# Kernel optimization log

Hardware: AMD Instinct MI355X
Metric: run time of the kernel (lower is better)

## Reference

```python
import jax, jax.numpy as jnp
import numpy as np

VOCAB = 50257
EMB = 256
HID = 256
FORGET_BIAS = 1.0


def setup_inputs() -> dict:
    key = jax.random.key(0)
    ks = jax.random.split(key, 8)
    B, T = 16, 256
    s = 0.05
    return {
        "tokens": jax.random.randint(ks[0], (B, T), 0, VOCAB, dtype=jnp.int32),
        # embedding matrix init mimics tf.random_uniform(-1, 1)
        "emb": jax.random.uniform(ks[1], (VOCAB, EMB), jnp.float32, -1.0, 1.0),
        "W1": jax.random.normal(ks[2], (EMB + HID, 4 * HID), jnp.float32) * s,
        "b1": jnp.zeros((4 * HID,), jnp.float32),
        "W2": jax.random.normal(ks[3], (HID + HID, 4 * HID), jnp.float32) * s,
        "b2": jnp.zeros((4 * HID,), jnp.float32),
        "Wout": jax.random.normal(ks[4], (HID, VOCAB), jnp.float32) * s,
        "bout": jnp.zeros((VOCAB,), jnp.float32),
    }


def _lstm_cell(c, h, x, W, b):
    # BasicLSTMCell: gates = [x, h] @ W + b, split i, j, f, o
    g = jnp.concatenate([x, h], axis=-1) @ W + b
    i, j, f, o = jnp.split(g, 4, axis=-1)
    c_new = c * jax.nn.sigmoid(f + FORGET_BIAS) + jax.nn.sigmoid(i) * jnp.tanh(j)
    h_new = jnp.tanh(c_new) * jax.nn.sigmoid(o)
    return c_new, h_new


def reference(tokens, emb, W1, b1, W2, b2, Wout, bout):
    B, T = tokens.shape
    x = emb[tokens]                 # [B, T, EMB] embedding lookup
    x_tm = jnp.swapaxes(x, 0, 1)    # [T, B, EMB] time-major for scan

    def step(carry, xt):
        c1, h1, c2, h2 = carry
        c1, h1 = _lstm_cell(c1, h1, xt, W1, b1)
        c2, h2 = _lstm_cell(c2, h2, h1, W2, b2)
        return (c1, h1, c2, h2), h2

    z = jnp.zeros((B, HID), x.dtype)
    _, hs = jax.lax.scan(step, (z, z, z, z), x_tm)  # hs: [T, B, HID]
    hs = jnp.swapaxes(hs, 0, 1).reshape(-1, HID)    # [B*T, HID] (batch-major flatten as in tf.reshape)
    logits = hs @ Wout + bout                        # [B*T, VOCAB]
    return logits
```

## Files before the change

kernel.cpp:

```cpp
#include <hip/hip_runtime.h>
#include <hip/hip_bf16.h>
#include <stdint.h>

#define BB 16
#define TT 256
#define HH 256
#define EE 256
#define GG 1024
#define VV 50257
#define NPAD 50688
#define NN 4096

typedef unsigned short u16;
typedef __attribute__((ext_vector_type(8))) short short8;
typedef __attribute__((ext_vector_type(4))) float f32x4;

__device__ __forceinline__ float sigm(float x){
    float e = __builtin_amdgcn_exp2f(fminf(-x*1.44269504f, 60.0f));
    return 1.0f/(1.0f+e);
}
__device__ __forceinline__ float tanha(float x){
    float e = __builtin_amdgcn_exp2f(fminf(x*2.885390082f, 60.0f));
    return (e-1.0f)/(e+1.0f);
}
__device__ __forceinline__ u16 f2bf(float f){
    uint32_t u = __float_as_uint(f);
    u = (u + 0x7FFFu + ((u>>16)&1u)) >> 16;
    return (u16)u;
}
__device__ __forceinline__ void st32_coh(uint32_t* p, uint32_t v){
    __hip_atomic_store(p, v, __ATOMIC_RELAXED, __HIP_MEMORY_SCOPE_AGENT);
}
__device__ __forceinline__ uint32_t poll_pair(const uint32_t* p){
    uint32_t v = __hip_atomic_load(p, __ATOMIC_RELAXED, __HIP_MEMORY_SCOPE_AGENT);
    while ((v & 0xFFFFu) == 0xFFFFu || (v >> 16) == 0xFFFFu){
        __builtin_amdgcn_s_sleep(1);
        v = __hip_atomic_load(p, __ATOMIC_RELAXED, __HIP_MEMORY_SCOPE_AGENT);
    }
    return v;
}
__device__ __forceinline__ void gl_lds16(const void* g, void* s){
    __builtin_amdgcn_global_load_lds((const __attribute__((address_space(1))) unsigned int*)g,
                                     (__attribute__((address_space(3))) unsigned int*)s, 16, 0, 0);
}

__global__ __launch_bounds__(256) void g1_kernel(const int* __restrict__ tok, const float* __restrict__ emb,
                                                 const float* __restrict__ W1, const float* __restrict__ b1,
                                                 float* __restrict__ G1t){
    __shared__ float xs[64*64];
    __shared__ float wsm[64*64];
    int n0 = blockIdx.x * 64;
    int g0 = blockIdx.y * 64;
    int tid = threadIdx.x;
    int sl = tid & 63;
    int kk = (tid >> 6) * 16;
    int mytok = tok[n0 + sl];
    float acc[4][4] = {};
    int ni = tid & 15, gi = tid >> 4;
    for (int kc = 0; kc < 4; ++kc){
        int k0 = kc*64;
        __syncthreads();
        #pragma unroll
        for (int i4 = 0; i4 < 4; ++i4){
            float4 xv = *(const float4*)(&emb[(size_t)mytok*EE + k0 + kk + i4*4]);
            xs[(kk+i4*4+0)*64 + sl] = xv.x;
            xs[(kk+i4*4+1)*64 + sl] = xv.y;
            xs[(kk+i4*4+2)*64 + sl] = xv.z;
            xs[(kk+i4*4+3)*64 + sl] = xv.w;
        }
        #pragma unroll
        for (int i = 0; i < 16; ++i){
            wsm[(kk+i)*64 + sl] = W1[(size_t)(k0+kk+i)*GG + g0 + sl];
        }
        __syncthreads();
        for (int k = 0; k < 64; ++k){
            float4 av = *(const float4*)(&xs[k*64 + ni*4]);
            float4 bv = *(const float4*)(&wsm[k*64 + gi*4]);
            float a_[4] = {av.x, av.y, av.z, av.w};
            float b_[4] = {bv.x, bv.y, bv.z, bv.w};
            #pragma unroll
            for (int i = 0; i < 4; ++i)
                #pragma unroll
                for (int j = 0; j < 4; ++j)
                    acc[i][j] += a_[i]*b_[j];
        }
    }
    #pragma unroll
    for (int i = 0; i < 4; ++i){
        int n = n0 + ni*4 + i;
        int b = n >> 8;
        int tt_ = n & 255;
        float4 o;
        o.x = acc[i][0] + b1[g0+gi*4+0];
        o.y = acc[i][1] + b1[g0+gi*4+1];
        o.z = acc[i][2] + b1[g0+gi*4+2];
        o.w = acc[i][3] + b1[g0+gi*4+3];
        *(float4*)(&G1t[(size_t)(tt_*16 + b)*GG + g0 + gi*4]) = o;
    }
}

__global__ __launch_bounds__(1024) void persist_kernel(
        const float* __restrict__ G1t, const float* __restrict__ W1,
        const float* __restrict__ W2, const float* __restrict__ b2,
        const float* __restrict__ Wout, u16* __restrict__ WoutT,
        u16* __restrict__ h1y, u16* __restrict__ h2b){
    __shared__ __align__(16) char smem[12288];
    const int bid = blockIdx.x;
    const int tid = threadIdx.x;

    if (bid >= 96){
        u16* tile = (u16*)smem;
        const int r = tid >> 4, i = tid & 15;
        for (int tau = bid - 96; tau < 792*4; tau += 128){
            int ky = tau / 792;
            int nx = tau - ky*792;
            int n0 = nx*64, k0 = ky*64;
            #pragma unroll
            for (int jj = 0; jj < 4; ++jj){
                int n = n0 + i*4 + jj;
                float f = (n < VV) ? Wout[(size_t)(k0 + r)*VV + n] : 0.0f;
                tile[(i*4 + jj)*66 + r] = f2bf(f);
            }
            __syncthreads();
            {
                int kl = i*4;
                uint2 v;
                v.x = (uint32_t)tile[r*66 + kl+0] | ((uint32_t)tile[r*66 + kl+1] << 16);
                v.y = (uint32_t)tile[r*66 + kl+2] | ((uint32_t)tile[r*66 + kl+3] << 16);
                *(uint2*)(&WoutT[(size_t)(n0 + r)*256 + k0 + kl]) = v;
            }
            __syncthreads();
        }
        return;
    }

    const int g  = bid & 7;
    const int rr = bid >> 3;
    const int l  = tid & 63;
    const int wv = tid >> 6;
    uint32_t* h1y32 = (uint32_t*)h1y;
    uint32_t* h2b32 = (uint32_t*)h2b;

    if (rr < 4){
        const int r1 = rr;
        const int gate = wv >> 2, usub = wv & 3;
        const int colw = gate*HH + 64*r1 + 16*usub;
        short8 wf[8];
        {
            const int col = colw + (l & 15);
            const int kb = (l >> 4) << 3;
            #pragma unroll
            for (int kk = 0; kk < 8; ++kk){
                short8 s;
                #pragma unroll
                for (int j = 0; j < 8; ++j)
                    s[j] = (short)f2bf(W1[(size_t)(HH + kk*32 + kb + j)*GG + col]);
                wf[kk] = s;
            }
        }
        u16*      hA   = (u16*)smem;
        uint32_t* hA32 = (uint32_t*)smem;
        float*    gm   = (float*)(smem + 1024);
        const int ab = tid >> 5, ap_ = tid & 31;
        float creg0 = 0.f, creg1 = 0.f;

        for (int t = 0; t < TT; ++t){
            float c0 = 0.f, c1 = 0.f;
            if (l < 16){
                c0 = G1t[((size_t)t*BB + 2*g + 0)*GG + colw + l];
                c1 = G1t[((size_t)t*BB + 2*g + 1)*GG + colw + l];
            }
            f32x4 acc = {c0, c1, 0.f, 0.f};
            if (t > 0){
                if (tid < 256){
                    int b = tid >> 7, p = tid & 127;
                    hA32[b*128 + p] = poll_pair(&h1y32[(((size_t)(t-1)*8 + g)*2 + b)*128 + p]);
                }
                __syncthreads();
                const u16* app = hA + (l & 1)*256 + ((l >> 4) << 3);
                f32x4 acc2 = {0.f, 0.f, 0.f, 0.f};
                #pragma unroll
                for (int kk = 0; kk < 4; ++kk){
                    acc  = __builtin_amdgcn_mfma_f32_16x16x32_bf16(*(const short8*)(app + (2*kk  )*32), wf[2*kk  ], acc , 0, 0, 0);
                    acc2 = __builtin_amdgcn_mfma_f32_16x16x32_bf16(*(const short8*)(app + (2*kk+1)*32), wf[2*kk+1], acc2, 0, 0, 0);
                }
                acc[0] += acc2[0];
                acc[1] += acc2[1];
            }
            if (l < 16){
                gm[(gate*64 + usub*16 + l)*2 + 0] = acc[0];
                gm[(gate*64 + usub*16 + l)*2 + 1] = acc[1];
            }
            __syncthreads();
            if (tid < 64){
                int u0 = 2*ap_, u1 = 2*ap_ + 1;
                float gi0 = gm[(0*64 + u0)*2 + ab], gi1 = gm[(0*64 + u1)*2 + ab];
                float gj0 = gm[(1*64 + u0)*2 + ab], gj1 = gm[(1*64 + u1)*2 + ab];
                float gf0 = gm[(2*64 + u0)*2 + ab], gf1 = gm[(2*64 + u1)*2 + ab];
                float go0 = gm[(3*64 + u0)*2 + ab], go1 = gm[(3*64 + u1)*2 + ab];
                float cn0 = creg0 * sigm(gf0 + 1.0f) + sigm(gi0)*tanha(gj0);
                float cn1 = creg1 * sigm(gf1 + 1.0f) + sigm(gi1)*tanha(gj1);
                float hn0 = tanha(cn0)*sigm(go0);
                float hn1 = tanha(cn1)*sigm(go1);
                creg0 = cn0; creg1 = cn1;
                uint32_t pk = (uint32_t)f2bf(hn0) | ((uint32_t)f2bf(hn1) << 16);
                st32_coh(&h1y32[(((size_t)t*8 + g)*2 + ab)*128 + 32*r1 + ap_], pk);
            }
            __syncthreads();
        }
    } else {
        const int r2 = rr - 4;
        const int nt = wv >> 1, kh = wv & 1;
        const int gate = nt >> 1, usub = nt & 1;
        const int colw = gate*HH + 32*r2 + 16*usub;
        short8 wf[8];
        {
            const int col = colw + (l & 15);
            const int kb = (l >> 4) << 3;
            #pragma unroll
            for (int kk = 0; kk < 8; ++kk){
                short8 s;
                #pragma unroll
                for (int j = 0; j < 8; ++j)
                    s[j] = (short)f2bf(W2[(size_t)(kh*256 + kk*32 + kb + j)*GG + col]);
                wf[kk] = s;
            }
        }
        u16*      uB   = (u16*)smem;
        uint32_t* uB32 = (uint32_t*)smem;
        float*    gm   = (float*)(smem + 2048);
        const int ab = tid >> 4, ap_ = tid & 15;
        float creg0 = 0.f, creg1 = 0.f;
        float bvs[4][2];
        if (tid < 32){
            #pragma unroll
            for (int gg = 0; gg < 4; ++gg){
                bvs[gg][0] = b2[gg*HH + 32*r2 + 2*ap_];
                bvs[gg][1] = b2[gg*HH + 32*r2 + 2*ap_ + 1];
            }
        }

        for (int tt = 0; tt < TT; ++tt){
            if (tid < 512){
                int b = tid >> 8, q = tid & 255;
                uint32_t v;
                if (q < 128)
                    v = poll_pair(&h1y32[(((size_t)tt*8 + g)*2 + b)*128 + q]);
                else if (tt > 0)
                    v = poll_pair(&h2b32[((size_t)(2*g + b)*TT + (tt-1))*128 + (q - 128)]);
                else
                    v = 0;
                uB32[b*256 + q] = v;
            }
            __syncthreads();
            f32x4 acc = {0.f, 0.f, 0.f, 0.f};
            f32x4 acc2 = {0.f, 0.f, 0.f, 0.f};
            const u16* app = uB + (l & 1)*512 + kh*256 + ((l >> 4) << 3);
            #pragma unroll
            for (int kk = 0; kk < 4; ++kk){
                acc  = __builtin_amdgcn_mfma_f32_16x16x32_bf16(*(const short8*)(app + (2*kk  )*32), wf[2*kk  ], acc , 0, 0, 0);
                acc2 = __builtin_amdgcn_mfma_f32_16x16x32_bf16(*(const short8*)(app + (2*kk+1)*32), wf[2*kk+1], acc2, 0, 0, 0);
            }
            acc[0] += acc2[0];
            acc[1] += acc2[1];
            if (l < 16){
                gm[((gate*32 + usub*16 + l)*2 + 0)*2 + kh] = acc[0];
                gm[((gate*32 + usub*16 + l)*2 + 1)*2 + kh] = acc[1];
            }
            __syncthreads();
            if (tid < 32){
                int u0 = 2*ap_, u1 = 2*ap_ + 1;
                float gi0 = gm[((0*32 + u0)*2 + ab)*2 + 0] + gm[((0*32 + u0)*2 + ab)*2 + 1] + bvs[0][0];
                float gi1 = gm[((0*32 + u1)*2 + ab)*2 + 0] + gm[((0*32 + u1)*2 + ab)*2 + 1] + bvs[0][1];
                float gj0 = gm[((1*32 + u0)*2 + ab)*2 + 0] + gm[((1*32 + u0)*2 + ab)*2 + 1] + bvs[1][0];
                float gj1 = gm[((1*32 + u1)*2 + ab)*2 + 0] + gm[((1*32 + u1)*2 + ab)*2 + 1] + bvs[1][1];
                float gf0 = gm[((2*32 + u0)*2 + ab)*2 + 0] + gm[((2*32 + u0)*2 + ab)*2 + 1] + bvs[2][0];
                float gf1 = gm[((2*32 + u1)*2 + ab)*2 + 0] + gm[((2*32 + u1)*2 + ab)*2 + 1] + bvs[2][1];
                float go0 = gm[((3*32 + u0)*2 + ab)*2 + 0] + gm[((3*32 + u0)*2 + ab)*2 + 1] + bvs[3][0];
                float go1 = gm[((3*32 + u1)*2 + ab)*2 + 0] + gm[((3*32 + u1)*2 + ab)*2 + 1] + bvs[3][1];
                float cn0 = creg0 * sigm(gf0 + 1.0f) + sigm(gi0)*tanha(gj0);
                float cn1 = creg1 * sigm(gf1 + 1.0f) + sigm(gi1)*tanha(gj1);
                float hn0 = tanha(cn0)*sigm(go0);
                float hn1 = tanha(cn1)*sigm(go1);
                creg0 = cn0; creg1 = cn1;
                uint32_t pk = (uint32_t)f2bf(hn0) | ((uint32_t)f2bf(hn1) << 16);
                st32_coh(&h2b32[((size_t)(2*g + ab)*TT + tt)*128 + 16*r2 + ap_], pk);
            }
            __syncthreads();
        }
    }
}

__global__ __launch_bounds__(512) void out_gemm(const u16* __restrict__ A, const u16* __restrict__ Bt,
                                                const float* __restrict__ bout, float* __restrict__ out){
    __shared__ __align__(16) char smem[36864];
    u16* ldsA = (u16*)smem;
    u16* ldsB = (u16*)(smem + 4096);
    float* gm  = (float*)smem;
    const int bid = blockIdx.x;
    const int x   = bid & 7;
    const int loc = bid >> 3;
    const int mb  = x*8 + (loc & 7);
    const int nb  = loc >> 3;
    const int m0 = mb*64, n0 = nb*512;
    const int tid = threadIdx.x;
    const int wv = tid >> 6, l = tid & 63;
    const int rg = wv >> 1;
    const int nh = wv & 1;
    const int lr = l & 15, lh = l >> 4;

    f32x4 acc[16];
    #pragma unroll
    for (int nf = 0; nf < 16; ++nf) acc[nf] = (f32x4){0.f,0.f,0.f,0.f};

    for (int ks = 0; ks < 8; ++ks){
        if (tid < 256){
            int f = tid, row = f >> 2, kp = f & 3;
            gl_lds16(A + (size_t)(m0+row)*256 + ks*32 + kp*8, (char*)ldsA + f*16);
        }
        #pragma unroll
        for (int j = 0; j < 4; ++j){
            int f = j*512 + tid, row = f >> 2, kp = f & 3;
            gl_lds16(Bt + (size_t)(n0+row)*256 + ks*32 + kp*8, (char*)ldsB + f*16);
        }
        __syncthreads();
        short8 af = *(const short8*)((const char*)ldsA + (rg*16+lr)*64 + lh*16);
        #pragma unroll
        for (int nf = 0; nf < 16; ++nf){
            int brow = nh*256 + nf*16 + lr;
            short8 bf = *(const short8*)((const char*)ldsB + brow*64 + lh*16);
            acc[nf] = __builtin_amdgcn_mfma_f32_16x16x32_bf16(af, bf, acc[nf], 0, 0, 0);
        }
        __syncthreads();
    }

    for (int c = 0; c < 4; ++c){
        if (rg == c){
            #pragma unroll
            for (int nf = 0; nf < 16; ++nf){
                int colL = nh*256 + nf*16 + lr;
                int gcol = n0 + colL;
                float bb = (gcol < VV) ? bout[gcol] : 0.0f;
                #pragma unroll
                for (int r = 0; r < 4; ++r)
                    gm[(lh*4 + r)*516 + colL] = acc[nf][r] + bb;
            }
        }
        __syncthreads();
        #pragma unroll
        for (int i = 0; i < 4; ++i){
            int idx = i*512 + tid;
            int row = idx >> 7;
            int c4 = (idx & 127) * 4;
            int gcol = n0 + c4;
            f32x4 v = *(const f32x4*)(gm + row*516 + c4);
            int grow = m0 + c*16 + row;
            if (gcol + 3 < VV){
                *(f32x4*)(&out[(size_t)grow*VV + gcol]) = v;
            } else {
                #pragma unroll
                for (int e = 0; e < 4; ++e)
                    if (gcol + e < VV) out[(size_t)grow*VV + gcol + e] = v[e];
            }
        }
        __syncthreads();
    }
}

extern "C" void kernel_launch(void* const* d_in, const int* in_sizes, int n_in,
                              void* d_out, int out_size, void* d_ws, size_t ws_size,
                              hipStream_t stream) {
    const int*   tok  = (const int*)d_in[0];
    const float* emb  = (const float*)d_in[1];
    const float* W1   = (const float*)d_in[2];
    const float* b1   = (const float*)d_in[3];
    const float* W2   = (const float*)d_in[4];
    const float* b2   = (const float*)d_in[5];
    const float* Wout = (const float*)d_in[6];
    const float* bout = (const float*)d_in[7];
    float* out = (float*)d_out;
    char* ws = (char*)d_ws;

    u16*   h1y   = (u16*)  (ws);
    u16*   h2b   = (u16*)  (ws + 2097152);
    float* G1t   = (float*)(ws + 4194304);
    u16*   WoutT = (u16*)  (ws + 20971520);

    hipMemsetAsync(ws, 0xFF, 4194304, stream);
    g1_kernel<<<dim3(64, 16), 256, 0, stream>>>(tok, emb, W1, b1, G1t);
    persist_kernel<<<224, 1024, 0, stream>>>(G1t, W1, W2, b2, Wout, WoutT, h1y, h2b);
    out_gemm<<<6336, 512, 0, stream>>>(h2b, WoutT, bout, out);
}
```

Measured before the change: 851.0 us.

## Overlap output GEMM with LSTM recurrence via flag-gated persistent workers

```diff
diff --git a/kernel.cpp b/kernel.cpp
--- a/kernel.cpp
+++ b/kernel.cpp
@@ -8,8 +8,9 @@
 #define EE 256
 #define GG 1024
 #define VV 50257
-#define NPAD 50688
 #define NN 4096
+#define NWK 352
+#define NTILE 12608
 
 typedef unsigned short u16;
 typedef __attribute__((ext_vector_type(8))) short short8;
@@ -99,86 +100,165 @@
     }
 }
 
-__global__ __launch_bounds__(1024) void persist_kernel(
+__global__ __launch_bounds__(256) void cast_transpose_wout(const float* __restrict__ Wout,
+                                                           u16* __restrict__ WoutT){
+    __shared__ u16 tile[64][65];
+    int n0 = blockIdx.x * 64;
+    int k0 = blockIdx.y * 64;
+    int tid = threadIdx.x;
+    int r  = tid >> 2;
+    int cq = tid & 3;
+    #pragma unroll
+    for (int i = 0; i < 16; ++i){
+        int n = n0 + cq*16 + i;
+        float v = (n < VV) ? Wout[(size_t)(k0 + r)*VV + n] : 0.0f;
+        tile[cq*16 + i][r] = f2bf(v);
+    }
+    __syncthreads();
+    #pragma unroll
+    for (int i4 = 0; i4 < 4; ++i4){
+        int kl = cq*16 + i4*4;
+        uint2 v;
+        v.x = (uint32_t)tile[r][kl+0] | ((uint32_t)tile[r][kl+1] << 16);
+        v.y = (uint32_t)tile[r][kl+2] | ((uint32_t)tile[r][kl+3] << 16);
+        *(uint2*)(&WoutT[(size_t)(n0 + r)*256 + k0 + kl]) = v;
+    }
+}
+
+__global__ __launch_bounds__(1024, 8) void fused_kernel(
         const float* __restrict__ G1t, const float* __restrict__ W1,
         const float* __restrict__ W2, const float* __restrict__ b2,
-        const float* __restrict__ Wout, u16* __restrict__ WoutT,
-        u16* __restrict__ h1y, u16* __restrict__ h2b){
-    __shared__ __align__(16) char smem[12288];
+        u16* __restrict__ h1y, u16* __restrict__ h2b,
+        const u16* __restrict__ Bt, const float* __restrict__ bout,
+        float* __restrict__ out, int* __restrict__ aflag){
+    __shared__ __align__(16) char smem[81920];
     const int bid = blockIdx.x;
     const int tid = threadIdx.x;
-
-    if (bid >= 96){
-        u16* tile = (u16*)smem;
-        const int r = tid >> 4, i = tid & 15;
-        for (int tau = bid - 96; tau < 792*4; tau += 128){
-            int ky = tau / 792;
-            int nx = tau - ky*792;
-            int n0 = nx*64, k0 = ky*64;
-            #pragma unroll
-            for (int jj = 0; jj < 4; ++jj){
-                int n = n0 + i*4 + jj;
-                float f = (n < VV) ? Wout[(size_t)(k0 + r)*VV + n] : 0.0f;
-                tile[(i*4 + jj)*66 + r] = f2bf(f);
-            }
-            __syncthreads();
-            {
-                int kl = i*4;
-                uint2 v;
-                v.x = (uint32_t)tile[r*66 + kl+0] | ((uint32_t)tile[r*66 + kl+1] << 16);
-                v.y = (uint32_t)tile[r*66 + kl+2] | ((uint32_t)tile[r*66 + kl+3] << 16);
-                *(uint2*)(&WoutT[(size_t)(n0 + r)*256 + k0 + kl]) = v;
-            }
-            __syncthreads();
-        }
-        return;
-    }
-
-    const int g  = bid & 7;
-    const int rr = bid >> 3;
-    const int l  = tid & 63;
-    const int wv = tid >> 6;
     uint32_t* h1y32 = (uint32_t*)h1y;
     uint32_t* h2b32 = (uint32_t*)h2b;
 
-    if (rr < 4){
-        const int r1 = rr;
-        const int gate = wv >> 2, usub = wv & 3;
-        const int colw = gate*HH + 64*r1 + 16*usub;
-        short8 wf[8];
-        {
-            const int col = colw + (l & 15);
-            const int kb = (l >> 4) << 3;
-            #pragma unroll
-            for (int kk = 0; kk < 8; ++kk){
-                short8 s;
-                #pragma unroll
-                for (int j = 0; j < 8; ++j)
-                    s[j] = (short)f2bf(W1[(size_t)(HH + kk*32 + kb + j)*GG + col]);
-                wf[kk] = s;
-            }
-        }
-        u16*      hA   = (u16*)smem;
-        uint32_t* hA32 = (uint32_t*)smem;
-        float*    gm   = (float*)(smem + 1024);
-        const int ab = tid >> 5, ap_ = tid & 31;
-        float creg0 = 0.f, creg1 = 0.f;
-
-        for (int t = 0; t < TT; ++t){
-            float c0 = 0.f, c1 = 0.f;
-            if (l < 16){
-                c0 = G1t[((size_t)t*BB + 2*g + 0)*GG + colw + l];
-                c1 = G1t[((size_t)t*BB + 2*g + 1)*GG + colw + l];
-            }
-            f32x4 acc = {c0, c1, 0.f, 0.f};
-            if (t > 0){
-                if (tid < 256){
-                    int b = tid >> 7, p = tid & 127;
-                    hA32[b*128 + p] = poll_pair(&h1y32[(((size_t)(t-1)*8 + g)*2 + b)*128 + p]);
+    if (bid < 96){
+        __builtin_amdgcn_s_setprio(1);
+        const int g  = bid & 7;
+        const int rr = bid >> 3;
+        const int l  = tid & 63;
+        const int wv = tid >> 6;
+
+        if (rr < 4){
+            const int r1 = rr;
+            const int gate = wv >> 2, usub = wv & 3;
+            const int colw = gate*HH + 64*r1 + 16*usub;
+            short8 wf[8];
+            {
+                const int col = colw + (l & 15);
+                const int kb = (l >> 4) << 3;
+                #pragma unroll
+                for (int kk = 0; kk < 8; ++kk){
+                    short8 s;
+                    #pragma unroll
+                    for (int j = 0; j < 8; ++j)
+                        s[j] = (short)f2bf(W1[(size_t)(HH + kk*32 + kb + j)*GG + col]);
+                    wf[kk] = s;
+                }
+            }
+            u16*      hA   = (u16*)smem;
+            uint32_t* hA32 = (uint32_t*)smem;
+            float*    gm   = (float*)(smem + 1024);
+            const int ab = tid >> 5, ap_ = tid & 31;
+            float creg0 = 0.f, creg1 = 0.f;
+
+            for (int t = 0; t < TT; ++t){
+                float c0 = 0.f, c1 = 0.f;
+                if (l < 16){
+                    c0 = G1t[((size_t)t*BB + 2*g + 0)*GG + colw + l];
+                    c1 = G1t[((size_t)t*BB + 2*g + 1)*GG + colw + l];
+                }
+                f32x4 acc = {c0, c1, 0.f, 0.f};
+                if (t > 0){
+                    if (tid < 256){
+                        int b = tid >> 7, p = tid & 127;
+                        hA32[b*128 + p] = poll_pair(&h1y32[(((size_t)(t-1)*8 + g)*2 + b)*128 + p]);
+                    }
+                    __syncthreads();
+                    const u16* app = hA + (l & 1)*256 + ((l >> 4) << 3);
+                    f32x4 acc2 = {0.f, 0.f, 0.f, 0.f};
+                    #pragma unroll
+                    for (int kk = 0; kk < 4; ++kk){
+                        acc  = __builtin_amdgcn_mfma_f32_16x16x32_bf16(*(const short8*)(app + (2*kk  )*32), wf[2*kk  ], acc , 0, 0, 0);
+                        acc2 = __builtin_amdgcn_mfma_f32_16x16x32_bf16(*(const short8*)(app + (2*kk+1)*32), wf[2*kk+1], acc2, 0, 0, 0);
+                    }
+                    acc[0] += acc2[0];
+                    acc[1] += acc2[1];
+                }
+                if (l < 16){
+                    gm[(gate*64 + usub*16 + l)*2 + 0] = acc[0];
+                    gm[(gate*64 + usub*16 + l)*2 + 1] = acc[1];
                 }
                 __syncthreads();
-                const u16* app = hA + (l & 1)*256 + ((l >> 4) << 3);
+                if (tid < 64){
+                    int u0 = 2*ap_, u1 = 2*ap_ + 1;
+                    float gi0 = gm[(0*64 + u0)*2 + ab], gi1 = gm[(0*64 + u1)*2 + ab];
+                    float gj0 = gm[(1*64 + u0)*2 + ab], gj1 = gm[(1*64 + u1)*2 + ab];
+                    float gf0 = gm[(2*64 + u0)*2 + ab], gf1 = gm[(2*64 + u1)*2 + ab];
+                    float go0 = gm[(3*64 + u0)*2 + ab], go1 = gm[(3*64 + u1)*2 + ab];
+                    float cn0 = creg0 * sigm(gf0 + 1.0f) + sigm(gi0)*tanha(gj0);
+                    float cn1 = creg1 * sigm(gf1 + 1.0f) + sigm(gi1)*tanha(gj1);
+                    float hn0 = tanha(cn0)*sigm(go0);
+                    float hn1 = tanha(cn1)*sigm(go1);
+                    creg0 = cn0; creg1 = cn1;
+                    uint32_t pk = (uint32_t)f2bf(hn0) | ((uint32_t)f2bf(hn1) << 16);
+                    st32_coh(&h1y32[(((size_t)t*8 + g)*2 + ab)*128 + 32*r1 + ap_], pk);
+                }
+                __syncthreads();
+            }
+        } else {
+            const int r2 = rr - 4;
+            const int nt = wv >> 1, kh = wv & 1;
+            const int gate = nt >> 1, usub = nt & 1;
+            const int colw = gate*HH + 32*r2 + 16*usub;
+            short8 wf[8];
+            {
+                const int col = colw + (l & 15);
+                const int kb = (l >> 4) << 3;
+                #pragma unroll
+                for (int kk = 0; kk < 8; ++kk){
+                    short8 s;
+                    #pragma unroll
+                    for (int j = 0; j < 8; ++j)
+                        s[j] = (short)f2bf(W2[(size_t)(kh*256 + kk*32 + kb + j)*GG + col]);
+                    wf[kk] = s;
+                }
+            }
+            u16*      uB   = (u16*)smem;
+            uint32_t* uB32 = (uint32_t*)smem;
+            float*    gm   = (float*)(smem + 2048);
+            const int ab = tid >> 4, ap_ = tid & 15;
+            float creg0 = 0.f, creg1 = 0.f;
+            float bvs[4][2];
+            if (tid < 32){
+                #pragma unroll
+                for (int gg = 0; gg < 4; ++gg){
+                    bvs[gg][0] = b2[gg*HH + 32*r2 + 2*ap_];
+                    bvs[gg][1] = b2[gg*HH + 32*r2 + 2*ap_ + 1];
+                }
+            }
+
+            for (int tt = 0; tt < TT; ++tt){
+                if (tid < 512){
+                    int b = tid >> 8, q = tid & 255;
+                    uint32_t v;
+                    if (q < 128)
+                        v = poll_pair(&h1y32[(((size_t)tt*8 + g)*2 + b)*128 + q]);
+                    else if (tt > 0)
+                        v = poll_pair(&h2b32[((size_t)(2*g + b)*TT + (tt-1))*128 + (q - 128)]);
+                    else
+                        v = 0;
+                    uB32[b*256 + q] = v;
+                }
+                __syncthreads();
+                f32x4 acc = {0.f, 0.f, 0.f, 0.f};
                 f32x4 acc2 = {0.f, 0.f, 0.f, 0.f};
+                const u16* app = uB + (l & 1)*512 + kh*256 + ((l >> 4) << 3);
                 #pragma unroll
                 for (int kk = 0; kk < 4; ++kk){
                     acc  = __builtin_amdgcn_mfma_f32_16x16x32_bf16(*(const short8*)(app + (2*kk  )*32), wf[2*kk  ], acc , 0, 0, 0);
@@ -186,185 +266,125 @@
                 }
                 acc[0] += acc2[0];
                 acc[1] += acc2[1];
-            }
-            if (l < 16){
-                gm[(gate*64 + usub*16 + l)*2 + 0] = acc[0];
-                gm[(gate*64 + usub*16 + l)*2 + 1] = acc[1];
+                if (l < 16){
+                    gm[((gate*32 + usub*16 + l)*2 + 0)*2 + kh] = acc[0];
+                    gm[((gate*32 + usub*16 + l)*2 + 1)*2 + kh] = acc[1];
+                }
+                __syncthreads();
+                if (tid < 32){
+                    int u0 = 2*ap_, u1 = 2*ap_ + 1;
+                    float gi0 = gm[((0*32 + u0)*2 + ab)*2 + 0] + gm[((0*32 + u0)*2 + ab)*2 + 1] + bvs[0][0];
+                    float gi1 = gm[((0*32 + u1)*2 + ab)*2 + 0] + gm[((0*32 + u1)*2 + ab)*2 + 1] + bvs[0][1];
+                    float gj0 = gm[((1*32 + u0)*2 + ab)*2 + 0] + gm[((1*32 + u0)*2 + ab)*2 + 1] + bvs[1][0];
+                    float gj1 = gm[((1*32 + u1)*2 + ab)*2 + 0] + gm[((1*32 + u1)*2 + ab)*2 + 1] + bvs[1][1];
+                    float gf0 = gm[((2*32 + u0)*2 + ab)*2 + 0] + gm[((2*32 + u0)*2 + ab)*2 + 1] + bvs[2][0];
+                    float gf1 = gm[((2*32 + u1)*2 + ab)*2 + 0] + gm[((2*32 + u1)*2 + ab)*2 + 1] + bvs[2][1];
+                    float go0 = gm[((3*32 + u0)*2 + ab)*2 + 0] + gm[((3*32 + u0)*2 + ab)*2 + 1] + bvs[3][0];
+                    float go1 = gm[((3*32 + u1)*2 + ab)*2 + 0] + gm[((3*32 + u1)*2 + ab)*2 + 1] + bvs[3][1];
+                    float cn0 = creg0 * sigm(gf0 + 1.0f) + sigm(gi0)*tanha(gj0);
+                    float cn1 = creg1 * sigm(gf1 + 1.0f) + sigm(gi1)*tanha(gj1);
+                    float hn0 = tanha(cn0)*sigm(go0);
+                    float hn1 = tanha(cn1)*sigm(go1);
+                    creg0 = cn0; creg1 = cn1;
+                    uint32_t pk = (uint32_t)f2bf(hn0) | ((uint32_t)f2bf(hn1) << 16);
+                    st32_coh(&h2b32[((size_t)(2*g + ab)*TT + tt)*128 + 16*r2 + ap_], pk);
+                }
+                __syncthreads();
+                if (((tt + 1) & 63) == 0 && tid < 32 && (tid & 15) == 0)
+                    __hip_atomic_fetch_add(&aflag[(2*g + (tid >> 4))*4 + (tt >> 6)], 1,
+                                           __ATOMIC_RELAXED, __HIP_MEMORY_SCOPE_AGENT);
+            }
+        }
+        return;
+    }
+
+    const int wid = bid - 96;
+    u16* ldsA[2] = {(u16*)smem,           (u16*)(smem + 8192)};
+    u16* ldsB[2] = {(u16*)(smem + 16384), (u16*)(smem + 49152)};
+    float* ldsF  = (float*)smem;
+    const int l = tid & 63, w = tid >> 6;
+    const int wm = w >> 2, wn = w & 3;
+    const int lr = l & 15, lh = l >> 4;
+    const u16* A = h2b;
+
+    #define WSTAGE(c, k0) { \
+        if (tid < 512){ \
+            int f = tid, row = f >> 3, kp = f & 7, kps = kp ^ (row & 7); \
+            gl_lds16(A + (size_t)(m0+row)*256 + (k0) + kps*8, (char*)ldsA[c] + f*16); \
+        } \
+        _Pragma("unroll") \
+        for (int j = 0; j < 2; ++j){ \
+            int f = j*1024 + tid, row = f >> 3, kp = f & 7, kps = kp ^ (row & 7); \
+            gl_lds16(Bt + (size_t)(n0+row)*256 + (k0) + kps*8, (char*)ldsB[c] + f*16); \
+        } }
+
+    for (int s = wid; s < NTILE; s += NWK){
+        const int q = s / 3152;
+        const int rem = s - q*3152;
+        const int nb = rem >> 4, b = rem & 15;
+        const int mb = b*4 + q;
+        const int m0 = mb*64, n0 = nb*256;
+
+        if (tid == 0){
+            while (__hip_atomic_load(&aflag[mb], __ATOMIC_RELAXED, __HIP_MEMORY_SCOPE_AGENT) < 8)
+                __builtin_amdgcn_s_sleep(32);
+            (void)__hip_atomic_load(&aflag[mb], __ATOMIC_ACQUIRE, __HIP_MEMORY_SCOPE_AGENT);
+        }
+        __syncthreads();
+
+        f32x4 acc[4];
+        #pragma unroll
+        for (int nf = 0; nf < 4; ++nf) acc[nf] = (f32x4){0.f,0.f,0.f,0.f};
+
+        WSTAGE(0, 0)
+        __syncthreads();
+        #pragma unroll
+        for (int ks = 0; ks < 4; ++ks){
+            const int cur = ks & 1;
+            if (ks < 3) WSTAGE(cur^1, (ks+1)*64)
+            #pragma unroll
+            for (int ksub = 0; ksub < 2; ++ksub){
+                const int kp = ksub*4 + lh;
+                int arow = wm*16 + lr;
+                short8 af = *(const short8*)((const char*)ldsA[cur] + arow*128 + ((kp ^ (arow&7)) << 4));
+                #pragma unroll
+                for (int nf = 0; nf < 4; ++nf){
+                    int brow = wn*64 + nf*16 + lr;
+                    short8 bf = *(const short8*)((const char*)ldsB[cur] + brow*128 + ((kp ^ (brow&7)) << 4));
+                    acc[nf] = __builtin_amdgcn_mfma_f32_16x16x32_bf16(af, bf, acc[nf], 0, 0, 0);
+                }
             }
             __syncthreads();
-            if (tid < 64){
-                int u0 = 2*ap_, u1 = 2*ap_ + 1;
-                float gi0 = gm[(0*64 + u0)*2 + ab], gi1 = gm[(0*64 + u1)*2 + ab];
-                float gj0 = gm[(1*64 + u0)*2 + ab], gj1 = gm[(1*64 + u1)*2 + ab];
-                float gf0 = gm[(2*64 + u0)*2 + ab], gf1 = gm[(2*64 + u1)*2 + ab];
-                float go0 = gm[(3*64 + u0)*2 + ab], go1 = gm[(3*64 + u1)*2 + ab];
-                float cn0 = creg0 * sigm(gf0 + 1.0f) + sigm(gi0)*tanha(gj0);
-                float cn1 = creg1 * sigm(gf1 + 1.0f) + sigm(gi1)*tanha(gj1);
-                float hn0 = tanha(cn0)*sigm(go0);
-                float hn1 = tanha(cn1)*sigm(go1);
-                creg0 = cn0; creg1 = cn1;
-                uint32_t pk = (uint32_t)f2bf(hn0) | ((uint32_t)f2bf(hn1) << 16);
-                st32_coh(&h1y32[(((size_t)t*8 + g)*2 + ab)*128 + 32*r1 + ap_], pk);
-            }
-            __syncthreads();
-        }
-    } else {
-        const int r2 = rr - 4;
-        const int nt = wv >> 1, kh = wv & 1;
-        const int gate = nt >> 1, usub = nt & 1;
-        const int colw = gate*HH + 32*r2 + 16*usub;
-        short8 wf[8];
-        {
-            const int col = colw + (l & 15);
-            const int kb = (l >> 4) << 3;
+        }
+
+        #pragma unroll
+        for (int nf = 0; nf < 4; ++nf){
+            int colL = wn*64 + nf*16 + lr;
+            int gcol = n0 + colL;
+            float bb = (gcol < VV) ? bout[gcol] : 0.0f;
             #pragma unroll
-            for (int kk = 0; kk < 8; ++kk){
-                short8 s;
-                #pragma unroll
-                for (int j = 0; j < 8; ++j)
-                    s[j] = (short)f2bf(W2[(size_t)(kh*256 + kk*32 + kb + j)*GG + col]);
-                wf[kk] = s;
-            }
-        }
-        u16*      uB   = (u16*)smem;
-        uint32_t* uB32 = (uint32_t*)smem;
-        float*    gm   = (float*)(smem + 2048);
-        const int ab = tid >> 4, ap_ = tid & 15;
-        float creg0 = 0.f, creg1 = 0.f;
-        float bvs[4][2];
-        if (tid < 32){
-            #pragma unroll
-            for (int gg = 0; gg < 4; ++gg){
-                bvs[gg][0] = b2[gg*HH + 32*r2 + 2*ap_];
-                bvs[gg][1] = b2[gg*HH + 32*r2 + 2*ap_ + 1];
-            }
-        }
-
-        for (int tt = 0; tt < TT; ++tt){
-            if (tid < 512){
-                int b = tid >> 8, q = tid & 255;
-                uint32_t v;
-                if (q < 128)
-                    v = poll_pair(&h1y32[(((size_t)tt*8 + g)*2 + b)*128 + q]);
-                else if (tt > 0)
-                    v = poll_pair(&h2b32[((size_t)(2*g + b)*TT + (tt-1))*128 + (q - 128)]);
-                else
-                    v = 0;
-                uB32[b*256 + q] = v;
-            }
-            __syncthreads();
-            f32x4 acc = {0.f, 0.f, 0.f, 0.f};
-            f32x4 acc2 = {0.f, 0.f, 0.f, 0.f};
-            const u16* app = uB + (l & 1)*512 + kh*256 + ((l >> 4) << 3);
-            #pragma unroll
-            for (int kk = 0; kk < 4; ++kk){
-                acc  = __builtin_amdgcn_mfma_f32_16x16x32_bf16(*(const short8*)(app + (2*kk  )*32), wf[2*kk  ], acc , 0, 0, 0);
-                acc2 = __builtin_amdgcn_mfma_f32_16x16x32_bf16(*(const short8*)(app + (2*kk+1)*32), wf[2*kk+1], acc2, 0, 0, 0);
-            }
-            acc[0] += acc2[0];
-            acc[1] += acc2[1];
-            if (l < 16){
-                gm[((gate*32 + usub*16 + l)*2 + 0)*2 + kh] = acc[0];
-                gm[((gate*32 + usub*16 + l)*2 + 1)*2 + kh] = acc[1];
-            }
-            __syncthreads();
-            if (tid < 32){
-                int u0 = 2*ap_, u1 = 2*ap_ + 1;
-                float gi0 = gm[((0*32 + u0)*2 + ab)*2 + 0] + gm[((0*32 + u0)*2 + ab)*2 + 1] + bvs[0][0];
-                float gi1 = gm[((0*32 + u1)*2 + ab)*2 + 0] + gm[((0*32 + u1)*2 + ab)*2 + 1] + bvs[0][1];
-                float gj0 = gm[((1*32 + u0)*2 + ab)*2 + 0] + gm[((1*32 + u0)*2 + ab)*2 + 1] + bvs[1][0];
-                float gj1 = gm[((1*32 + u1)*2 + ab)*2 + 0] + gm[((1*32 + u1)*2 + ab)*2 + 1] + bvs[1][1];
-                float gf0 = gm[((2*32 + u0)*2 + ab)*2 + 0] + gm[((2*32 + u0)*2 + ab)*2 + 1] + bvs[2][0];
-                float gf1 = gm[((2*32 + u1)*2 + ab)*2 + 0] + gm[((2*32 + u1)*2 + ab)*2 + 1] + bvs[2][1];
-                float go0 = gm[((3*32 + u0)*2 + ab)*2 + 0] + gm[((3*32 + u0)*2 + ab)*2 + 1] + bvs[3][0];
-                float go1 = gm[((3*32 + u1)*2 + ab)*2 + 0] + gm[((3*32 + u1)*2 + ab)*2 + 1] + bvs[3][1];
-                float cn0 = creg0 * sigm(gf0 + 1.0f) + sigm(gi0)*tanha(gj0);
-                float cn1 = creg1 * sigm(gf1 + 1.0f) + sigm(gi1)*tanha(gj1);
-                float hn0 = tanha(cn0)*sigm(go0);
-                float hn1 = tanha(cn1)*sigm(go1);
-                creg0 = cn0; creg1 = cn1;
-                uint32_t pk = (uint32_t)f2bf(hn0) | ((uint32_t)f2bf(hn1) << 16);
-                st32_coh(&h2b32[((size_t)(2*g + ab)*TT + tt)*128 + 16*r2 + ap_], pk);
-            }
-            __syncthreads();
-        }
-    }
-}
-
-__global__ __launch_bounds__(512) void out_gemm(const u16* __restrict__ A, const u16* __restrict__ Bt,
-                                                const float* __restrict__ bout, float* __restrict__ out){
-    __shared__ __align__(16) char smem[36864];
-    u16* ldsA = (u16*)smem;
-    u16* ldsB = (u16*)(smem + 4096);
-    float* gm  = (float*)smem;
-    const int bid = blockIdx.x;
-    const int x   = bid & 7;
-    const int loc = bid >> 3;
-    const int mb  = x*8 + (loc & 7);
-    const int nb  = loc >> 3;
-    const int m0 = mb*64, n0 = nb*512;
-    const int tid = threadIdx.x;
-    const int wv = tid >> 6, l = tid & 63;
-    const int rg = wv >> 1;
-    const int nh = wv & 1;
-    const int lr = l & 15, lh = l >> 4;
-
-    f32x4 acc[16];
-    #pragma unroll
-    for (int nf = 0; nf < 16; ++nf) acc[nf] = (f32x4){0.f,0.f,0.f,0.f};
-
-    for (int ks = 0; ks < 8; ++ks){
-        if (tid < 256){
-            int f = tid, row = f >> 2, kp = f & 3;
-            gl_lds16(A + (size_t)(m0+row)*256 + ks*32 + kp*8, (char*)ldsA + f*16);
-        }
+            for (int r = 0; r < 4; ++r)
+                ldsF[(wm*16 + lh*4 + r)*256 + colL] = acc[nf][r] + bb;
+        }
+        __syncthreads();
         #pragma unroll
         for (int j = 0; j < 4; ++j){
-            int f = j*512 + tid, row = f >> 2, kp = f & 3;
-            gl_lds16(Bt + (size_t)(n0+row)*256 + ks*32 + kp*8, (char*)ldsB + f*16);
-        }
-        __syncthreads();
-        short8 af = *(const short8*)((const char*)ldsA + (rg*16+lr)*64 + lh*16);
-        #pragma unroll
-        for (int nf = 0; nf < 16; ++nf){
-            int brow = nh*256 + nf*16 + lr;
-            short8 bf = *(const short8*)((const char*)ldsB + brow*64 + lh*16);
-            acc[nf] = __builtin_amdgcn_mfma_f32_16x16x32_bf16(af, bf, acc[nf], 0, 0, 0);
-        }
-        __syncthreads();
-    }
-
-    for (int c = 0; c < 4; ++c){
-        if (rg == c){
-            #pragma unroll
-            for (int nf = 0; nf < 16; ++nf){
-                int colL = nh*256 + nf*16 + lr;
-                int gcol = n0 + colL;
-                float bb = (gcol < VV) ? bout[gcol] : 0.0f;
-                #pragma unroll
-                for (int r = 0; r < 4; ++r)
-                    gm[(lh*4 + r)*516 + colL] = acc[nf][r] + bb;
-            }
-        }
-        __syncthreads();
-        #pragma unroll
-        for (int i = 0; i < 4; ++i){
-            int idx = i*512 + tid;
-            int row = idx >> 7;
-            int c4 = (idx & 127) * 4;
+            int f = j*1024 + tid;
+            int row = f >> 6;
+            int c4 = (f & 63)*4;
             int gcol = n0 + c4;
-            f32x4 v = *(const f32x4*)(gm + row*516 + c4);
-            int grow = m0 + c*16 + row;
+            f32x4 v = *(const f32x4*)(ldsF + row*256 + c4);
             if (gcol + 3 < VV){
-                *(f32x4*)(&out[(size_t)grow*VV + gcol]) = v;
+                *(f32x4*)(&out[(size_t)(m0+row)*VV + gcol]) = v;
             } else {
                 #pragma unroll
                 for (int e = 0; e < 4; ++e)
-                    if (gcol + e < VV) out[(size_t)grow*VV + gcol + e] = v[e];
-            }
-        }
-        __syncthreads();
-    }
+                    if (gcol + e < VV) out[(size_t)(m0+row)*VV + gcol + e] = v[e];
+            }
+        }
+        __syncthreads();
+    }
+    #undef WSTAGE
 }
 
 extern "C" void kernel_launch(void* const* d_in, const int* in_sizes, int n_in,
@@ -381,13 +401,16 @@
     float* out = (float*)d_out;
     char* ws = (char*)d_ws;
 
-    u16*   h1y   = (u16*)  (ws);
-    u16*   h2b   = (u16*)  (ws + 2097152);
-    float* G1t   = (float*)(ws + 4194304);
-    u16*   WoutT = (u16*)  (ws + 20971520);
-
-    hipMemsetAsync(ws, 0xFF, 4194304, stream);
+    int*   aflag = (int*)  (ws);
+    u16*   h1y   = (u16*)  (ws + 4096);
+    u16*   h2b   = (u16*)  (ws + 4096 + 2097152);
+    float* G1t   = (float*)(ws + 4096 + 4194304);
+    u16*   WoutT = (u16*)  (ws + 4096 + 20971520);
+
+    hipMemsetAsync(ws, 0, 4096, stream);
+    hipMemsetAsync(ws + 4096, 0xFF, 4194304, stream);
     g1_kernel<<<dim3(64, 16), 256, 0, stream>>>(tok, emb, W1, b1, G1t);
-    persist_kernel<<<224, 1024, 0, stream>>>(G1t, W1, W2, b2, Wout, WoutT, h1y, h2b);
-    out_gemm<<<6336, 512, 0, stream>>>(h2b, WoutT, bout, out);
-}
+    cast_transpose_wout<<<dim3(792, 4), 256, 0, stream>>>(Wout, WoutT);
+    fused_kernel<<<96 + NWK, 1024, 0, stream>>>(G1t, W1, W2, b2, h1y, h2b,
+                                                WoutT, bout, out, aflag);
+}
```

Result: slower. 943.6 us (+10.9%).
